# Performance work log

Hardware: AMD Instinct MI355X
Metric: run time of the kernel (lower is better)

Reference implementation:

```python
import jax, jax.numpy as jnp
import numpy as np

B, N, D, H, S = 64, 1000, 512, 8, 20
DK = D // H
TANH_CLIP = 10.0
NEG = -1e9


def setup_inputs() -> dict:
    key = jax.random.key(0)
    k1, k2, k3, k4, k5 = jax.random.split(key, 5)
    embeddings = jax.random.normal(k1, (B, N, D), dtype=jnp.float32)
    q = jax.random.normal(k2, (B, S, D), dtype=jnp.float32)
    # action_mask: True = feasible. Ensure at least one feasible node per row.
    action_mask = jax.random.bernoulli(k3, 0.5, (B, S, N))
    action_mask = action_mask.at[:, :, 0].set(True)
    W_kvl = jax.random.normal(k4, (D, 3 * D), dtype=jnp.float32) * (1.0 / np.sqrt(D))
    W_out = jax.random.normal(k5, (D, D), dtype=jnp.float32) * (1.0 / np.sqrt(D))
    return {"embeddings": embeddings, "q": q, "action_mask": action_mask,
            "W_kvl": W_kvl, "W_out": W_out}


def reference(embeddings, q, action_mask, W_kvl, W_out):
    # _precompute: project node embeddings into glimpse K, V and logit K
    kvl = jnp.einsum('bnd,de->bne', embeddings, W_kvl)  # [B,N,3D]
    glimpse_k, glimpse_v, logit_k = jnp.split(kvl, 3, axis=-1)
    # dynamic embedding is zero (StaticEmbedding for TSP)

    mask = ~action_mask  # True = infeasible, shape [B,S,N]

    # multi-head glimpse attention
    qh = q.reshape(B, S, H, DK)
    kh = glimpse_k.reshape(B, N, H, DK)
    vh = glimpse_v.reshape(B, N, H, DK)
    compat = jnp.einsum('bshd,bnhd->bhsn', qh, kh) / np.sqrt(DK)
    compat = jnp.where(mask[:, None, :, :], NEG, compat)
    attn = jax.nn.softmax(compat, axis=-1)
    heads = jnp.einsum('bhsn,bnhd->bshd', attn, vh).reshape(B, S, D)
    glimpse = jnp.einsum('bsd,de->bse', heads, W_out)  # [B,S,D]

    # pointer logits against logit_k, tanh clipping, mask, log-softmax
    logits = jnp.einsum('bsd,bnd->bsn', glimpse, logit_k) / np.sqrt(D)
    logits = TANH_CLIP * jnp.tanh(logits)
    logits = jnp.where(mask, NEG, logits)
    log_p = jax.nn.log_softmax(logits, axis=-1)  # [B,S,N]

    # rearrange 'b s l -> (s b) l'
    return jnp.swapaxes(log_p, 0, 1).reshape(S * B, N)
```

## Files before the change

### kernel.cpp

```cpp
#include <hip/hip_runtime.h>

#define BB 64
#define NN 1000
#define NP 1024
#define DD 512
#define HH 8
#define SS 20
#define NEGV -1e9f

typedef float v4f __attribute__((ext_vector_type(4)));
typedef short v8s __attribute__((ext_vector_type(8)));
typedef int   v8i __attribute__((ext_vector_type(8)));
typedef int   v4i __attribute__((ext_vector_type(4)));
typedef unsigned char uchar;
typedef unsigned long long ulong_t;

static __device__ __forceinline__ short f2bf(float f) {
    unsigned u = __builtin_bit_cast(unsigned, f);
    u = (u + 0x7fffu + ((u >> 16) & 1u)) >> 16;
    return (short)u;
}
static __device__ __forceinline__ float bf2f(short s) {
    unsigned u = ((unsigned)(unsigned short)s) << 16;
    return __builtin_bit_cast(float, u);
}
static __device__ __forceinline__ uchar f2fp8(float f) {
    return (uchar)(__builtin_amdgcn_cvt_pk_fp8_f32(f, 0.f, 0, false) & 0xff);
}

static __device__ __forceinline__ void gld16(const void* g, void* l) {
    __builtin_amdgcn_global_load_lds(
        (const __attribute__((address_space(1))) void*)(g),
        (__attribute__((address_space(3))) void*)(l),
        16, 0, 0);
}

__global__ void prep(const float* __restrict__ Wkvl, uchar* __restrict__ Wt8,
                     const float* __restrict__ Wout, short* __restrict__ Wot,
                     const float* __restrict__ emb, int* __restrict__ emb8) {
    __shared__ float t[32][33];
    int bid = blockIdx.x, tid = threadIdx.x;
    if (bid < 768) {
        int c0 = (bid % 48) * 32, r0 = (bid / 48) * 32;
        int x = tid & 31, y = tid >> 5;
        for (int k = 0; k < 32; k += 8)
            t[y + k][x] = Wkvl[(long)(r0 + y + k) * 1536 + c0 + x];
        __syncthreads();
        for (int k = 0; k < 32; k += 8)
            Wt8[(long)(c0 + y + k) * 512 + r0 + x] = f2fp8(t[x][y + k]);
    } else if (bid < 1024) {
        int bb = bid - 768;
        int c0 = (bb & 15) * 32, r0 = (bb >> 4) * 32;
        int x = tid & 31, y = tid >> 5;
        for (int k = 0; k < 32; k += 8)
            t[y + k][x] = Wout[(long)(r0 + y + k) * 512 + c0 + x];
        __syncthreads();
        for (int k = 0; k < 32; k += 8)
            Wot[(long)(c0 + y + k) * 512 + r0 + x] = f2bf(t[x][y + k]);
    } else {
        int i = (bid - 1024) * 256 + tid;
        long o = (long)i * 8;
        v4f a = *(const v4f*)(emb + o);
        v4f b = *(const v4f*)(emb + o + 4);
        int lo = __builtin_amdgcn_cvt_pk_fp8_f32(a.x, a.y, 0, false);
        lo = __builtin_amdgcn_cvt_pk_fp8_f32(a.z, a.w, lo, true);
        int hi = __builtin_amdgcn_cvt_pk_fp8_f32(b.x, b.y, 0, false);
        hi = __builtin_amdgcn_cvt_pk_fp8_f32(b.z, b.w, hi, true);
        int2 r; r.x = lo; r.y = hi;
        *(int2*)(emb8 + i * 2) = r;
    }
}

__global__ __launch_bounds__(256) void gemm_kvl(const uchar* __restrict__ emb8,
                                                const uchar* __restrict__ Wt8,
                                                uchar* __restrict__ kvl8) {
    __shared__ __align__(16) uchar As[128 * 128];
    __shared__ __align__(16) uchar Bs[128 * 128];
    int tid = threadIdx.x;
    int id = blockIdx.x;
    int m_idx, n_idx;
    if (id < 5952) { int g = id / 96, r = id % 96; m_idx = g * 8 + (r & 7); n_idx = r >> 3; }
    else { int t = id - 5952; m_idx = 496 + (t & 3); n_idx = t >> 2; }
    int n0 = n_idx * 128, m0 = m_idx * 128;
    int wid = tid >> 6, lane = tid & 63, quad = lane >> 4, l16 = lane & 15;
    int wm = wid & 1, wn = wid >> 1;
    v4f acc[4][4] = {};
    const uchar* Ag = emb8 + (long)m0 * 512;
    const uchar* Bg = Wt8 + (long)n0 * 512;
    int rsub = lane >> 3;
    int kc = ((lane & 7) ^ rsub) * 16;
    for (int kk = 0; kk < 512; kk += 128) {
        #pragma unroll
        for (int p = 0; p < 4; ++p) {
            int rl = wid * 32 + p * 8;
            gld16(Ag + (long)(rl + rsub) * 512 + kk + kc, As + rl * 128);
            gld16(Bg + (long)(rl + rsub) * 512 + kk + kc, Bs + rl * 128);
        }
        __syncthreads();
        v8i af[4], bf[4];
        #pragma unroll
        for (int i = 0; i < 4; ++i) {
            int m = wm * 64 + i * 16 + l16;
            int c0 = (quad * 2) ^ (m & 7), c1 = (quad * 2 + 1) ^ (m & 7);
            v4i lo = *(const v4i*)(As + m * 128 + c0 * 16);
            v4i hi = *(const v4i*)(As + m * 128 + c1 * 16);
            af[i] = __builtin_shufflevector(lo, hi, 0, 1, 2, 3, 4, 5, 6, 7);
        }
        #pragma unroll
        for (int j = 0; j < 4; ++j) {
            int n = wn * 64 + j * 16 + l16;
            int c0 = (quad * 2) ^ (n & 7), c1 = (quad * 2 + 1) ^ (n & 7);
            v4i lo = *(const v4i*)(Bs + n * 128 + c0 * 16);
            v4i hi = *(const v4i*)(Bs + n * 128 + c1 * 16);
            bf[j] = __builtin_shufflevector(lo, hi, 0, 1, 2, 3, 4, 5, 6, 7);
        }
        #pragma unroll
        for (int i = 0; i < 4; ++i)
            #pragma unroll
            for (int j = 0; j < 4; ++j)
                acc[i][j] = __builtin_amdgcn_mfma_scale_f32_16x16x128_f8f6f4(
                    af[i], bf[j], acc[i][j], 0, 0, 0, 0x7f7f7f7f, 0, 0x7f7f7f7f);
        __syncthreads();
    }
    short* rp = (short*)As;
    short* r = rp + wid * (16 * 72);
    #pragma unroll
    for (int i = 0; i < 4; ++i) {
        #pragma unroll
        for (int j = 0; j < 4; ++j)
            #pragma unroll
            for (int rr = 0; rr < 4; ++rr)
                r[(quad * 4 + rr) * 72 + j * 16 + l16] = f2bf(acc[i][j][rr]);
        #pragma unroll
        for (int h = 0; h < 2; ++h) {
            int rowl = h * 8 + (lane >> 3);
            int colc = (lane & 7) * 8;
            v8s val = *(const v8s*)(r + rowl * 72 + colc);
            int lo = __builtin_amdgcn_cvt_pk_fp8_f32(bf2f(val[0]), bf2f(val[1]), 0, false);
            lo = __builtin_amdgcn_cvt_pk_fp8_f32(bf2f(val[2]), bf2f(val[3]), lo, true);
            int hi = __builtin_amdgcn_cvt_pk_fp8_f32(bf2f(val[4]), bf2f(val[5]), 0, false);
            hi = __builtin_amdgcn_cvt_pk_fp8_f32(bf2f(val[6]), bf2f(val[7]), hi, true);
            int2 st; st.x = lo; st.y = hi;
            *(int2*)(kvl8 + (long)(m0 + wm * 64 + i * 16 + rowl) * 1536 +
                     n0 + wn * 64 + colc) = st;
        }
    }
}

__global__ void transpose_v(const uchar* __restrict__ kvl8, uchar* __restrict__ Vt8) {
    int bh = blockIdx.x, b = bh >> 3, h = bh & 7;
    int n0 = blockIdx.y * 64;
    __shared__ uchar T[64][72];
    int tid = threadIdx.x;
    #pragma unroll
    for (int it = 0; it < 2; ++it) {
        int nl = (tid >> 3) + it * 32;
        int n = n0 + nl;
        int nc = n < NN ? n : NN - 1;
        int d0 = (tid & 7) * 8;
        ulong_t v = *(const ulong_t*)(kvl8 + ((long)b * NN + nc) * 1536 + DD + h * 64 + d0);
        uchar* vb = (uchar*)&v;
        #pragma unroll
        for (int j = 0; j < 8; ++j) T[d0 + j][nl] = vb[j];
    }
    __syncthreads();
    #pragma unroll
    for (int it = 0; it < 2; ++it) {
        int d = (tid >> 3) + it * 32;
        int ns = (tid & 7) * 8;
        *(ulong_t*)(Vt8 + ((long)bh * 64 + d) * NP + n0 + ns) = *(const ulong_t*)&T[d][ns];
    }
}

#define CST 1036
__global__ __launch_bounds__(512) void attn_fused(const float* __restrict__ q,
                                                  const uchar* __restrict__ kvl8,
                                                  const uchar* __restrict__ Vt8,
                                                  const int* __restrict__ mask,
                                                  float* __restrict__ heads) {
    int b = blockIdx.x, h = blockIdx.y;
    __shared__ __align__(16) uchar qs[32 * 72];
    __shared__ __align__(16) short cmp[SS * CST];
    int tid = threadIdx.x, wid = tid >> 6, lane = tid & 63, quad = lane >> 4, l16 = lane & 15;
    for (int i = tid; i < 32 * 64; i += 512) {
        int row = i >> 6, col = i & 63;
        float v = (row < SS) ? q[((long)b * SS + row) * DD + h * 64 + col] : 0.f;
        qs[row * 72 + col] = f2fp8(v);
    }
    __syncthreads();
    long af[2][2];
    #pragma unroll
    for (int mt = 0; mt < 2; ++mt)
        #pragma unroll
        for (int ks = 0; ks < 2; ++ks)
            af[mt][ks] = *(const long*)(qs + (mt * 16 + l16) * 72 + ks * 32 + quad * 8);
    for (int t = 0; t < 8; ++t) {
        int nt = wid * 8 + t;
        int n = nt * 16 + l16;
        int nc = n < NN ? n : NN - 1;
        const uchar* kp = kvl8 + ((long)b * NN + nc) * 1536 + h * 64 + quad * 8;
        long b0 = *(const long*)kp;
        long b1 = *(const long*)(kp + 32);
        #pragma unroll
        for (int mt = 0; mt < 2; ++mt) {
            v4f a = {};
            a = __builtin_amdgcn_mfma_f32_16x16x32_fp8_fp8(af[mt][0], b0, a, 0, 0, 0);
            a = __builtin_amdgcn_mfma_f32_16x16x32_fp8_fp8(af[mt][1], b1, a, 0, 0, 0);
            #pragma unroll
            for (int r = 0; r < 4; ++r) {
                int s = mt * 16 + quad * 4 + r;
                if (s < SS) cmp[s * CST + nt * 16 + l16] = f2bf(a[r] * 0.125f);
            }
        }
    }
    __syncthreads();
    for (int s = wid; s < SS; s += 8) {
        const int* mr = mask + ((long)b * SS + s) * NN;
        float x[16];
        float mx = NEGV;
        #pragma unroll
        for (int i = 0; i < 16; ++i) {
            int n = lane + 64 * i;
            float v = bf2f(cmp[s * CST + n]);
            bool feas = (n < NN) && (mr[n < NN ? n : 0] != 0);
            x[i] = feas ? v : NEGV;
            mx = fmaxf(mx, x[i]);
        }
        for (int off = 32; off; off >>= 1) mx = fmaxf(mx, __shfl_xor(mx, off));
        float sum = 0.f;
        #pragma unroll
        for (int i = 0; i < 16; ++i) { x[i] = __expf(x[i] - mx); sum += x[i]; }
        for (int off = 32; off; off >>= 1) sum += __shfl_xor(sum, off);
        float inv = 1.0f / sum;
        uchar* pr = (uchar*)cmp + (long)s * (CST * 2);
        #pragma unroll
        for (int i = 0; i < 16; ++i) pr[lane + 64 * i] = f2fp8(x[i] * inv);
    }
    __syncthreads();
    int mt = wid & 1, dt = wid >> 1;
    int srow = mt * 16 + l16; if (srow > SS - 1) srow = SS - 1;
    const uchar* ap = (const uchar*)cmp + (long)srow * (CST * 2) + quad * 8;
    const uchar* vb = Vt8 + (long)(b * HH + h) * 64 * NP;
    v4f acc = {};
    for (int k0 = 0; k0 < NP; k0 += 32) {
        long afr = *(const long*)(ap + k0);
        long bfr = *(const long*)(vb + (long)(dt * 16 + l16) * NP + k0 + quad * 8);
        acc = __builtin_amdgcn_mfma_f32_16x16x32_fp8_fp8(afr, bfr, acc, 0, 0, 0);
    }
    #pragma unroll
    for (int r = 0; r < 4; ++r) {
        int s = mt * 16 + quad * 4 + r;
        if (s < SS)
            heads[((long)b * SS + s) * DD + h * 64 + dt * 16 + l16] = acc[r];
    }
}

__global__ __launch_bounds__(256) void out_proj(const float* __restrict__ heads,
                                                const short* __restrict__ Wot,
                                                float* __restrict__ glimpse) {
    __shared__ __align__(16) short As[64 * 40], Bs[64 * 40];
    int tid = threadIdx.x;
    int m0 = blockIdx.x * 64, n0 = blockIdx.y * 64;
    int wid = tid >> 6, lane = tid & 63, quad = lane >> 4, l16 = lane & 15;
    int wm = wid & 1, wn = wid >> 1;
    int arow = tid >> 3, akol = (tid & 7) * 4;
    int brow = tid >> 2, bkol = (tid & 3) * 8;
    v4f acc[2][2] = {};
    for (int kk = 0; kk < 512; kk += 32) {
        #pragma unroll
        for (int p = 0; p < 2; ++p) {
            int r = arow + p * 32;
            v4f a = *(const v4f*)(heads + (long)(m0 + r) * 512 + kk + akol);
            short4 s4;
            s4.x = f2bf(a.x); s4.y = f2bf(a.y); s4.z = f2bf(a.z); s4.w = f2bf(a.w);
            *(short4*)(As + r * 40 + akol) = s4;
        }
        *(uint4*)(Bs + brow * 40 + bkol) =
            *(const uint4*)(Wot + (long)(n0 + brow) * 512 + kk + bkol);
        __syncthreads();
        #pragma unroll
        for (int i = 0; i < 2; ++i) {
            v8s af = *(const v8s*)(As + (wm * 32 + i * 16 + l16) * 40 + quad * 8);
            #pragma unroll
            for (int j = 0; j < 2; ++j) {
                v8s bf = *(const v8s*)(Bs + (wn * 32 + j * 16 + l16) * 40 + quad * 8);
                acc[i][j] = __builtin_amdgcn_mfma_f32_16x16x32_bf16(af, bf, acc[i][j], 0, 0, 0);
            }
        }
        __syncthreads();
    }
    #pragma unroll
    for (int i = 0; i < 2; ++i)
        #pragma unroll
        for (int j = 0; j < 2; ++j)
            #pragma unroll
            for (int r = 0; r < 4; ++r)
                glimpse[(long)(m0 + wm * 32 + i * 16 + quad * 4 + r) * 512 +
                        n0 + wn * 32 + j * 16 + l16] = acc[i][j][r];
}

__global__ __launch_bounds__(256) void ptr_logits(const float* __restrict__ glimpse,
                                                  const uchar* __restrict__ kvl8,
                                                  float* __restrict__ logits) {
    int b = blockIdx.x, g = blockIdx.y;
    __shared__ __align__(16) uchar Gs[32 * 520];
    int tid = threadIdx.x;
    #pragma unroll
    for (int it = 0; it < 16; ++it) {
        int e = it * 1024 + tid * 4;
        int row = e >> 9, col = e & 511;
        int pk = 0;
        if (row < SS) {
            v4f a = *(const v4f*)(glimpse + ((long)b * SS + row) * 512 + col);
            pk = __builtin_amdgcn_cvt_pk_fp8_f32(a.x, a.y, 0, false);
            pk = __builtin_amdgcn_cvt_pk_fp8_f32(a.z, a.w, pk, true);
        }
        *(int*)(Gs + row * 520 + col) = pk;
    }
    __syncthreads();
    int wid = tid >> 6, lane = tid & 63, quad = lane >> 4, l16 = lane & 15;
    const float scale = 0.04419417382415922f;
    int nt = g * 4 + wid;
    int n = nt * 16 + l16;
    int ncl = n < NN ? n : NN - 1;
    const uchar* kp = kvl8 + ((long)b * NN + ncl) * 1536 + 1024 + quad * 8;
    v4f acc[2] = {};
    for (int k = 0; k < 16; ++k) {
        long bfr = *(const long*)(kp + k * 32);
        #pragma unroll
        for (int m = 0; m < 2; ++m) {
            long afr = *(const long*)(Gs + (m * 16 + l16) * 520 + k * 32 + quad * 8);
            acc[m] = __builtin_amdgcn_mfma_f32_16x16x32_fp8_fp8(afr, bfr, acc[m], 0, 0, 0);
        }
    }
    #pragma unroll
    for (int m = 0; m < 2; ++m)
        #pragma unroll
        for (int r = 0; r < 4; ++r) {
            int s = m * 16 + quad * 4 + r;
            if (s < SS)
                logits[((long)b * SS + s) * NP + nt * 16 + l16] = acc[m][r] * scale;
        }
}

__global__ __launch_bounds__(256) void logsoftmax_out(const float* __restrict__ logits,
                                                      const int* __restrict__ mask,
                                                      float* __restrict__ out) {
    int row = blockIdx.x;
    int b = row / SS, s = row % SS;
    int tid = threadIdx.x;
    __shared__ float red[8];
    int n0 = tid * 4;
    v4f v = *(const v4f*)(logits + (long)row * NP + n0);
    const int* mr = mask + (long)row * NN;
    float x[4];
    float mx = NEGV;
    #pragma unroll
    for (int j = 0; j < 4; ++j) {
        int n = n0 + j;
        float t = 10.f * tanhf(v[j]);
        bool feas = (n < NN) && (mr[n < NN ? n : 0] != 0);
        x[j] = feas ? t : NEGV;
        mx = fmaxf(mx, x[j]);
    }
    for (int off = 32; off; off >>= 1) mx = fmaxf(mx, __shfl_xor(mx, off));
    int wid = tid >> 6, lane = tid & 63;
    if (lane == 0) red[wid] = mx;
    __syncthreads();
    mx = fmaxf(fmaxf(red[0], red[1]), fmaxf(red[2], red[3]));
    float sum = 0.f;
    #pragma unroll
    for (int j = 0; j < 4; ++j) sum += __expf(x[j] - mx);
    for (int off = 32; off; off >>= 1) sum += __shfl_xor(sum, off);
    __syncthreads();
    if (lane == 0) red[4 + wid] = sum;
    __syncthreads();
    sum = red[4] + red[5] + red[6] + red[7];
    float lse = mx + __logf(sum);
    float* orow = out + ((long)s * BB + b) * NN;
    #pragma unroll
    for (int j = 0; j < 4; ++j) {
        int n = n0 + j;
        if (n < NN) orow[n] = x[j] - lse;
    }
}

extern "C" void kernel_launch(void* const* d_in, const int* in_sizes, int n_in,
                              void* d_out, int out_size, void* d_ws, size_t ws_size,
                              hipStream_t stream) {
    const float* emb  = (const float*)d_in[0];
    const float* q    = (const float*)d_in[1];
    const int*   mask = (const int*)d_in[2];
    const float* Wkvl = (const float*)d_in[3];
    const float* Wout = (const float*)d_in[4];
    float* out = (float*)d_out;

    char* ws = (char*)d_ws;
    uchar* kvl8    = (uchar*)ws; ws += (size_t)64000 * 1536;
    uchar* Vt8     = (uchar*)ws; ws += (size_t)512 * 64 * NP;
    uchar* Wt8     = (uchar*)ws; ws += (size_t)1536 * 512;
    uchar* emb8    = (uchar*)ws; ws += (size_t)64000 * 512;
    short* Wot     = (short*)ws; ws += (size_t)512 * 512 * 2;
    float* heads   = (float*)ws; ws += (size_t)BB * SS * DD * 4;
    float* glimpse = (float*)ws; ws += (size_t)BB * SS * DD * 4;
    float* logits  = (float*)ws; ws += (size_t)BB * SS * NP * 4;

    prep<<<dim3(1024 + 16000), 256, 0, stream>>>(Wkvl, Wt8, Wout, Wot, emb, (int*)emb8);
    gemm_kvl<<<dim3(6000), 256, 0, stream>>>(emb8, Wt8, kvl8);
    transpose_v<<<dim3(512, 16), 256, 0, stream>>>(kvl8, Vt8);
    attn_fused<<<dim3(BB, HH), 512, 0, stream>>>(q, kvl8, Vt8, mask, heads);
    out_proj<<<dim3(20, 8), 256, 0, stream>>>(heads, Wot, glimpse);
    ptr_logits<<<dim3(BB, 16), 256, 0, stream>>>(glimpse, kvl8, logits);
    logsoftmax_out<<<dim3(BB * SS), 256, 0, stream>>>(logits, mask, out);
}
```

Baseline: 353.3 us.

## Enlarge KVL GEMM tiles to 256x256 with double-buffered LDS and XCD-aware mapping

Rewrites the fp8 projection GEMM to use 256x256 output tiles computed by 512 threads. It adds a 128 KB double-buffered dynamic LDS buffer so the next K-slice loads during MFMA work, interleaved with barriers and s_setprio raises around the MFMA groups. Blocks are remapped so that contiguous tile ranges land on the same XCD, aiming for better L2 reuse. The larger per-block LDS limits residency to one block per CU, and the extra barriers add sync overhead in exchange for more operand reuse and overlap.

```diff
diff --git a/kernel.cpp b/kernel.cpp
--- a/kernel.cpp
+++ b/kernel.cpp
@@ -71,66 +71,112 @@
     }
 }
 
-__global__ __launch_bounds__(256) void gemm_kvl(const uchar* __restrict__ emb8,
-                                                const uchar* __restrict__ Wt8,
-                                                uchar* __restrict__ kvl8) {
-    __shared__ __align__(16) uchar As[128 * 128];
-    __shared__ __align__(16) uchar Bs[128 * 128];
+__global__ __launch_bounds__(512, 2) void gemm_kvl(const uchar* __restrict__ emb8,
+                                                   const uchar* __restrict__ Wt8,
+                                                   uchar* __restrict__ kvl8) {
+    extern __shared__ __align__(16) uchar smem[];
+    uchar* As0 = smem;
+    uchar* Bs0 = smem + 65536;
     int tid = threadIdx.x;
     int id = blockIdx.x;
-    int m_idx, n_idx;
-    if (id < 5952) { int g = id / 96, r = id % 96; m_idx = g * 8 + (r & 7); n_idx = r >> 3; }
-    else { int t = id - 5952; m_idx = 496 + (t & 3); n_idx = t >> 2; }
-    int n0 = n_idx * 128, m0 = m_idx * 128;
+    int xcd = id & 7, j0 = id >> 3;
+    int wgid = (xcd < 4 ? xcd * 188 : 752 + (xcd - 4) * 187) + j0;
+    int m_idx = wgid / 6, n_idx = wgid - m_idx * 6;
+    int m0 = m_idx * 256, n0 = n_idx * 256;
     int wid = tid >> 6, lane = tid & 63, quad = lane >> 4, l16 = lane & 15;
     int wm = wid & 1, wn = wid >> 1;
-    v4f acc[4][4] = {};
     const uchar* Ag = emb8 + (long)m0 * 512;
     const uchar* Bg = Wt8 + (long)n0 * 512;
     int rsub = lane >> 3;
     int kc = ((lane & 7) ^ rsub) * 16;
-    for (int kk = 0; kk < 512; kk += 128) {
-        #pragma unroll
-        for (int p = 0; p < 4; ++p) {
-            int rl = wid * 32 + p * 8;
-            gld16(Ag + (long)(rl + rsub) * 512 + kk + kc, As + rl * 128);
-            gld16(Bg + (long)(rl + rsub) * 512 + kk + kc, Bs + rl * 128);
-        }
+
+    v4f acc[8][4] = {};
+
+    auto stage2 = [&](int bi, int kk, int p) {
+        int rl = wid * 32 + p * 8;
+        gld16(Ag + (long)(rl + rsub) * 512 + kk + kc, As0 + bi * 32768 + rl * 128);
+        gld16(Bg + (long)(rl + rsub) * 512 + kk + kc, Bs0 + bi * 32768 + rl * 128);
+    };
+    auto ldfrag = [&](const uchar* base, int row) -> v8i {
+        int c0 = (quad * 2) ^ (row & 7);
+        v4i lo = *(const v4i*)(base + row * 128 + c0 * 16);
+        v4i hi = *(const v4i*)(base + row * 128 + (c0 ^ 1) * 16);
+        return __builtin_shufflevector(lo, hi, 0, 1, 2, 3, 4, 5, 6, 7);
+    };
+
+    #pragma unroll
+    for (int p = 0; p < 4; ++p) stage2(0, 0, p);
+    __syncthreads();
+
+    v8i af[4], bf[4];
+    for (int t = 0; t < 4; ++t) {
+        int cur = t & 1;
+        const uchar* ab = As0 + cur * 32768;
+        const uchar* bb = Bs0 + cur * 32768;
+        int kn = (t + 1) * 128;
+        #pragma unroll
+        for (int i = 0; i < 4; ++i) af[i] = ldfrag(ab, wm * 128 + i * 16 + l16);
+        #pragma unroll
+        for (int jj = 0; jj < 2; ++jj) bf[jj] = ldfrag(bb, wn * 64 + jj * 16 + l16);
+        if (t < 3) stage2(cur ^ 1, kn, 0);
+        __builtin_amdgcn_s_barrier();
+        __builtin_amdgcn_s_setprio(1);
+        #pragma unroll
+        for (int i = 0; i < 4; ++i)
+            #pragma unroll
+            for (int jj = 0; jj < 2; ++jj)
+                acc[i][jj] = __builtin_amdgcn_mfma_scale_f32_16x16x128_f8f6f4(
+                    af[i], bf[jj], acc[i][jj], 0, 0, 0, 0x7f7f7f7f, 0, 0x7f7f7f7f);
+        __builtin_amdgcn_s_setprio(0);
+        __builtin_amdgcn_s_barrier();
+        #pragma unroll
+        for (int jj = 2; jj < 4; ++jj) bf[jj] = ldfrag(bb, wn * 64 + jj * 16 + l16);
+        if (t < 3) stage2(cur ^ 1, kn, 1);
+        __builtin_amdgcn_s_barrier();
+        __builtin_amdgcn_s_setprio(1);
+        #pragma unroll
+        for (int i = 0; i < 4; ++i)
+            #pragma unroll
+            for (int jj = 2; jj < 4; ++jj)
+                acc[i][jj] = __builtin_amdgcn_mfma_scale_f32_16x16x128_f8f6f4(
+                    af[i], bf[jj], acc[i][jj], 0, 0, 0, 0x7f7f7f7f, 0, 0x7f7f7f7f);
+        __builtin_amdgcn_s_setprio(0);
+        __builtin_amdgcn_s_barrier();
+        #pragma unroll
+        for (int i = 0; i < 4; ++i) af[i] = ldfrag(ab, wm * 128 + (i + 4) * 16 + l16);
+        if (t < 3) stage2(cur ^ 1, kn, 2);
+        __builtin_amdgcn_s_barrier();
+        __builtin_amdgcn_s_setprio(1);
+        #pragma unroll
+        for (int i = 0; i < 4; ++i)
+            #pragma unroll
+            for (int jj = 0; jj < 2; ++jj)
+                acc[i + 4][jj] = __builtin_amdgcn_mfma_scale_f32_16x16x128_f8f6f4(
+                    af[i], bf[jj], acc[i + 4][jj], 0, 0, 0, 0x7f7f7f7f, 0, 0x7f7f7f7f);
+        __builtin_amdgcn_s_setprio(0);
+        __builtin_amdgcn_s_barrier();
+        if (t < 3) stage2(cur ^ 1, kn, 3);
+        __builtin_amdgcn_s_barrier();
+        __builtin_amdgcn_s_setprio(1);
+        #pragma unroll
+        for (int i = 0; i < 4; ++i)
+            #pragma unroll
+            for (int jj = 2; jj < 4; ++jj)
+                acc[i + 4][jj] = __builtin_amdgcn_mfma_scale_f32_16x16x128_f8f6f4(
+                    af[i], bf[jj], acc[i + 4][jj], 0, 0, 0, 0x7f7f7f7f, 0, 0x7f7f7f7f);
+        __builtin_amdgcn_s_setprio(0);
         __syncthreads();
-        v8i af[4], bf[4];
-        #pragma unroll
-        for (int i = 0; i < 4; ++i) {
-            int m = wm * 64 + i * 16 + l16;
-            int c0 = (quad * 2) ^ (m & 7), c1 = (quad * 2 + 1) ^ (m & 7);
-            v4i lo = *(const v4i*)(As + m * 128 + c0 * 16);
-            v4i hi = *(const v4i*)(As + m * 128 + c1 * 16);
-            af[i] = __builtin_shufflevector(lo, hi, 0, 1, 2, 3, 4, 5, 6, 7);
-        }
-        #pragma unroll
-        for (int j = 0; j < 4; ++j) {
-            int n = wn * 64 + j * 16 + l16;
-            int c0 = (quad * 2) ^ (n & 7), c1 = (quad * 2 + 1) ^ (n & 7);
-            v4i lo = *(const v4i*)(Bs + n * 128 + c0 * 16);
-            v4i hi = *(const v4i*)(Bs + n * 128 + c1 * 16);
-            bf[j] = __builtin_shufflevector(lo, hi, 0, 1, 2, 3, 4, 5, 6, 7);
-        }
-        #pragma unroll
-        for (int i = 0; i < 4; ++i)
-            #pragma unroll
-            for (int j = 0; j < 4; ++j)
-                acc[i][j] = __builtin_amdgcn_mfma_scale_f32_16x16x128_f8f6f4(
-                    af[i], bf[j], acc[i][j], 0, 0, 0, 0x7f7f7f7f, 0, 0x7f7f7f7f);
-        __syncthreads();
-    }
-    short* rp = (short*)As;
+    }
+
+    short* rp = (short*)smem;
     short* r = rp + wid * (16 * 72);
     #pragma unroll
-    for (int i = 0; i < 4; ++i) {
-        #pragma unroll
-        for (int j = 0; j < 4; ++j)
+    for (int i = 0; i < 8; ++i) {
+        #pragma unroll
+        for (int jj = 0; jj < 4; ++jj)
             #pragma unroll
             for (int rr = 0; rr < 4; ++rr)
-                r[(quad * 4 + rr) * 72 + j * 16 + l16] = f2bf(acc[i][j][rr]);
+                r[(quad * 4 + rr) * 72 + jj * 16 + l16] = f2bf(acc[i][jj][rr]);
         #pragma unroll
         for (int h = 0; h < 2; ++h) {
             int rowl = h * 8 + (lane >> 3);
@@ -141,7 +187,7 @@
             int hi = __builtin_amdgcn_cvt_pk_fp8_f32(bf2f(val[4]), bf2f(val[5]), 0, false);
             hi = __builtin_amdgcn_cvt_pk_fp8_f32(bf2f(val[6]), bf2f(val[7]), hi, true);
             int2 st; st.x = lo; st.y = hi;
-            *(int2*)(kvl8 + (long)(m0 + wm * 64 + i * 16 + rowl) * 1536 +
+            *(int2*)(kvl8 + (long)(m0 + wm * 128 + i * 16 + rowl) * 1536 +
                      n0 + wn * 64 + colc) = st;
         }
     }
@@ -405,8 +451,15 @@
     float* glimpse = (float*)ws; ws += (size_t)BB * SS * DD * 4;
     float* logits  = (float*)ws; ws += (size_t)BB * SS * NP * 4;
 
+    static int s_attr_done = 0;
+    if (!s_attr_done) {
+        hipFuncSetAttribute(reinterpret_cast<const void*>(gemm_kvl),
+                            hipFuncAttributeMaxDynamicSharedMemorySize, 131072);
+        s_attr_done = 1;
+    }
+
     prep<<<dim3(1024 + 16000), 256, 0, stream>>>(Wkvl, Wt8, Wout, Wot, emb, (int*)emb8);
-    gemm_kvl<<<dim3(6000), 256, 0, stream>>>(emb8, Wt8, kvl8);
+    gemm_kvl<<<dim3(1500), 512, 131072, stream>>>(emb8, Wt8, kvl8);
     transpose_v<<<dim3(512, 16), 256, 0, stream>>>(kvl8, Vt8);
     attn_fused<<<dim3(BB, HH), 512, 0, stream>>>(q, kvl8, Vt8, mask, heads);
     out_proj<<<dim3(20, 8), 256, 0, stream>>>(heads, Wot, glimpse);
```

Result: slower. 361.0 us (+2.2%).
